# Kernel optimization log

Measured on AMD Instinct MI355X. Metric: run time of the kernel, lower is better.

The kernel has to match this reference:

```python
import jax, jax.numpy as jnp
import numpy as np

B, S, H = 8, 8192, 1024
CAPACITY_FACTOR = 0.5


def setup_inputs() -> dict:
    key = jax.random.key(0)
    ks = jax.random.split(key, 5)
    sc = lambda fan: np.float32(1.0 / np.sqrt(fan))
    return {
        "x": jax.random.normal(ks[0], (B, S, H), dtype=jnp.float32),
        # router: Linear(H, H//4) -> ReLU -> Linear(H//4, 1)
        "W1": jax.random.normal(ks[1], (H, H // 4), dtype=jnp.float32) * sc(H),
        "b1": jnp.zeros((H // 4,), dtype=jnp.float32),
        "W2": jax.random.normal(ks[2], (H // 4, 1), dtype=jnp.float32) * sc(H // 4),
        "b2": jnp.zeros((1,), dtype=jnp.float32),
        # external layer_fn realized as a dense layer: gelu(x @ Wl)
        "Wl": jax.random.normal(ks[3], (H, H), dtype=jnp.float32) * sc(H),
    }


def reference(x, W1, b1, W2, b2, Wl):
    # router scores [B, S, 1]
    scores = jax.nn.relu(jnp.einsum("bsh,hd->bsd", x, W1) + b1)
    scores = jnp.einsum("bsd,do->bso", scores, W2) + b2
    routing_weights = jax.nn.sigmoid(scores)  # [B, S, 1]

    # eval path: process only top-capacity tokens per batch row
    capacity = int(S * CAPACITY_FACTOR)
    _, top_idx = jax.lax.top_k(scores[..., 0], capacity)  # [B, C]

    selected = jnp.take_along_axis(x, top_idx[..., None], axis=1)  # [B, C, H]
    processed = jax.nn.gelu(jnp.einsum("bch,hd->bcd", selected, Wl))  # layer_fn

    batch_idx = jnp.arange(x.shape[0])[:, None]  # [B, 1]
    output = x.at[batch_idx, top_idx].set(processed)  # scatter back into clone of x
    return output, routing_weights
```

## Files before the change

kernel.cpp:

```cpp
#include <hip/hip_runtime.h>
#include <stdint.h>

#define B_   8
#define S_   8192
#define H_   1024
#define HQ_  256
#define CAP_ 4096
#define UCAP_ (S_-CAP_)
#define M_   (B_*CAP_)
#define EPSB 0.012f
#define LCAP 8192

using f32x4 = __attribute__((ext_vector_type(4))) float;
using s16x8 = __attribute__((ext_vector_type(8))) short;

__device__ __forceinline__ unsigned short f2bf(float f) {
  unsigned u = __float_as_uint(f);
  u += 0x7FFF + ((u >> 16) & 1);
  return (unsigned short)(u >> 16);
}
__device__ __forceinline__ float bf2f(unsigned short h) {
  return __uint_as_float(((unsigned)h) << 16);
}

__device__ __forceinline__ float gelu_f(float v) {
  float s = v + 0.044715f * v * v * v;
  float e = __expf(-1.5957691216057308f * s);
  return v * __builtin_amdgcn_rcpf(1.0f + e);
}

__device__ __forceinline__ unsigned mono(float f) {
  unsigned u = __float_as_uint(f);
  return (u & 0x80000000u) ? ~u : (u | 0x80000000u);
}
__device__ __forceinline__ float unmono(unsigned k) {
  unsigned u = (k & 0x80000000u) ? (k & 0x7fffffffu) : ~k;
  return __uint_as_float(u);
}

__device__ __forceinline__ void gload_lds16(const void* g, void* l) {
  __builtin_amdgcn_global_load_lds(
      (const __attribute__((address_space(1))) void*)(uintptr_t)g,
      (__attribute__((address_space(3))) void*)(uintptr_t)l,
      16, 0, 0);
}

__global__ __launch_bounds__(256) void prep_w1_kernel(
    const float* __restrict__ W1, unsigned short* __restrict__ w1t_hi) {
  __shared__ float tile[32][33];
  const int n0 = blockIdx.x * 32, k0 = blockIdx.y * 32;
  const int tx = threadIdx.x, ty = threadIdx.y;
  for (int i = ty; i < 32; i += 8) tile[i][tx] = W1[(size_t)(k0 + i) * HQ_ + n0 + tx];
  __syncthreads();
  for (int i = ty; i < 32; i += 8)
    w1t_hi[(size_t)(n0 + i) * H_ + k0 + tx] = f2bf(tile[tx][i]);
}

__global__ __launch_bounds__(512) void router_mfma_kernel(
    const float* __restrict__ x, const unsigned short* __restrict__ w1t_hi,
    const float* __restrict__ b1, const float* __restrict__ W2,
    const float* __restrict__ b2, float* __restrict__ scores) {
  __shared__ __align__(16) unsigned short AsH[128 * 32];
  __shared__ __align__(16) unsigned short BsH[256 * 32];
  __shared__ float part[128][4];
  const int t = threadIdx.x;
  const int lane = t & 63, w = t >> 6;
  const int m0 = blockIdx.x * 128;
  const int wr = w >> 2, wc = w & 3;
  const int r16 = lane & 15, ks = lane >> 4;

  f32x4 acc[4][4];
  #pragma unroll
  for (int i = 0; i < 4; ++i)
    #pragma unroll
    for (int j = 0; j < 4; ++j) acc[i][j] = (f32x4){0.f, 0.f, 0.f, 0.f};

  for (int k0 = 0; k0 < H_; k0 += 32) {
    #pragma unroll
    for (int u = 0; u < 2; ++u) {
      int idx = t + u * 512;
      int row = idx >> 3, q = idx & 7;
      float4 v = *(const float4*)&x[(size_t)(m0 + row) * H_ + k0 + q * 4];
      ushort4 hh;
      hh.x = f2bf(v.x); hh.y = f2bf(v.y); hh.z = f2bf(v.z); hh.w = f2bf(v.w);
      int so = row * 32 + (((q >> 1) ^ (row & 3)) << 3) + (q & 1) * 4;
      *(ushort4*)&AsH[so] = hh;
    }
    {
      int c0 = w * 64;
      #pragma unroll
      for (int q = 0; q < 2; ++q) {
        int cc0 = (q * 8 + w) * 64;
        int g = cc0 + lane;
        int row = g >> 2, sl = g & 3;
        int slz = sl ^ (row & 3);
        gload_lds16(&w1t_hi[(size_t)row * H_ + k0 + slz * 8], &BsH[cc0 * 8]);
      }
      (void)c0;
    }
    __syncthreads();
    s16x8 ah[4], bh[4];
    #pragma unroll
    for (int i = 0; i < 4; ++i) {
      int r = wr * 64 + i * 16 + r16;
      int co = (ks ^ (r & 3)) * 8;
      ah[i] = *(const s16x8*)&AsH[r * 32 + co];
    }
    #pragma unroll
    for (int j = 0; j < 4; ++j) {
      int r = wc * 64 + j * 16 + r16;
      int co = (ks ^ (r & 3)) * 8;
      bh[j] = *(const s16x8*)&BsH[r * 32 + co];
    }
    #pragma unroll
    for (int i = 0; i < 4; ++i)
      #pragma unroll
      for (int j = 0; j < 4; ++j)
        acc[i][j] = __builtin_amdgcn_mfma_f32_16x16x32_bf16(ah[i], bh[j], acc[i][j], 0, 0, 0);
    __syncthreads();
  }

  float b1v[4], w2v[4];
  #pragma unroll
  for (int j = 0; j < 4; ++j) {
    int n = wc * 64 + j * 16 + r16;
    b1v[j] = b1[n]; w2v[j] = W2[n];
  }
  const int g4 = lane >> 4;
  #pragma unroll
  for (int i = 0; i < 4; ++i) {
    #pragma unroll
    for (int r = 0; r < 4; ++r) {
      float p = 0.f;
      #pragma unroll
      for (int j = 0; j < 4; ++j) {
        float h = acc[i][j][r] + b1v[j];
        h = fmaxf(h, 0.f);
        p = fmaf(h, w2v[j], p);
      }
      p += __shfl_xor(p, 1);
      p += __shfl_xor(p, 2);
      p += __shfl_xor(p, 4);
      p += __shfl_xor(p, 8);
      if (r16 == 0) part[wr * 64 + i * 16 + g4 * 4 + r][wc] = p;
    }
  }
  __syncthreads();
  if (t < 128)
    scores[m0 + t] = part[t][0] + part[t][1] + part[t][2] + part[t][3] + b2[0];
}

__global__ __launch_bounds__(1024) void select_kernel(
    const float* __restrict__ scores, float* __restrict__ thr) {
  __shared__ unsigned hist[2048];
  __shared__ unsigned sh_b, sh_gt;
  const int b = blockIdx.x;
  const int tid = threadIdx.x;
  const float* srow = scores + (size_t)b * S_;
  unsigned prefix = 0; int plen = 0; unsigned rank = CAP_;
  #pragma unroll
  for (int round = 0; round < 3; ++round) {
    const int nb = (round < 2) ? 11 : 10;
    hist[tid] = 0; hist[tid + 1024] = 0;
    __syncthreads();
    for (int i = tid; i < S_; i += 1024) {
      unsigned k = mono(srow[i]);
      if (plen == 0 || (k >> (32 - plen)) == prefix) {
        unsigned bucket = (k << plen) >> (32 - nb);
        atomicAdd(&hist[bucket], 1u);
      }
    }
    __syncthreads();
    for (int s = 1; s < 2048; s <<= 1) {
      unsigned t0 = (tid + s < 2048) ? hist[tid + s] : 0;
      unsigned t1 = (tid + 1024 + s < 2048) ? hist[tid + 1024 + s] : 0;
      __syncthreads();
      hist[tid] += t0; hist[tid + 1024] += t1;
      __syncthreads();
    }
    #pragma unroll
    for (int h = 0; h < 2; ++h) {
      int i = tid + h * 1024;
      unsigned ge = hist[i];
      unsigned gt = (i < 2047) ? hist[i + 1] : 0;
      if (gt < rank && rank <= ge) { sh_b = (unsigned)i; sh_gt = gt; }
    }
    __syncthreads();
    prefix = (prefix << nb) | sh_b;
    plen += nb;
    rank -= sh_gt;
    __syncthreads();
  }
  if (tid == 0) thr[b] = unmono(prefix);
}

__global__ __launch_bounds__(256) void band_kernel(
    const float* __restrict__ scores, const float* __restrict__ thr,
    int* __restrict__ list, int* __restrict__ count) {
  int i = blockIdx.x * 256 + threadIdx.x;
  float s = scores[i];
  int b = i >> 13;
  if (fabsf(s - thr[b]) <= EPSB) {
    int p = atomicAdd(count, 1);
    if (p < LCAP) list[p] = i;
  }
}

__global__ __launch_bounds__(256) void recompute_kernel(
    const float* __restrict__ x, const float* __restrict__ W1,
    const float* __restrict__ b1, const float* __restrict__ W2,
    const float* __restrict__ b2, const int* __restrict__ list,
    const int* __restrict__ count, float* __restrict__ scores) {
  __shared__ float xr[4][H_];
  __shared__ float red[4][4];
  int n = *count; if (n > LCAP) n = LCAP;
  const int j = threadIdx.x;
  for (int base = blockIdx.x * 4; base < n; base += gridDim.x * 4) {
    int nt = n - base; if (nt > 4) nt = 4;
    for (int tt = 0; tt < 4; ++tt) {
      int tok = list[base + ((tt < nt) ? tt : 0)];
      const float* xrow = x + (size_t)tok * H_;
      for (int k = j; k < H_; k += 256) xr[tt][k] = xrow[k];
    }
    __syncthreads();
    float a0 = 0.f, a1 = 0.f, a2 = 0.f, a3 = 0.f;
    for (int k = 0; k < H_; ++k) {
      float wv = W1[(size_t)k * HQ_ + j];
      a0 = fmaf(xr[0][k], wv, a0);
      a1 = fmaf(xr[1][k], wv, a1);
      a2 = fmaf(xr[2][k], wv, a2);
      a3 = fmaf(xr[3][k], wv, a3);
    }
    float aa[4] = {a0, a1, a2, a3};
    #pragma unroll
    for (int tt = 0; tt < 4; ++tt) {
      float h = fmaxf(aa[tt] + b1[j], 0.f);
      float v = h * W2[j];
      v += __shfl_xor(v, 1);  v += __shfl_xor(v, 2);  v += __shfl_xor(v, 4);
      v += __shfl_xor(v, 8);  v += __shfl_xor(v, 16); v += __shfl_xor(v, 32);
      if ((j & 63) == 0) red[tt][j >> 6] = v;
    }
    __syncthreads();
    if (j < nt)
      scores[list[base + j]] = red[j][0] + red[j][1] + red[j][2] + red[j][3] + b2[0];
    __syncthreads();
  }
}

__global__ __launch_bounds__(1024) void compact_kernel(
    const float* __restrict__ scores, const float* __restrict__ thr,
    int* __restrict__ comp, int* __restrict__ ucomp) {
  __shared__ int wc_eq[16], wc_sel[16], red[16];
  const int b = blockIdx.x;
  const float T = thr[b];
  const float* srow = scores + (size_t)b * S_;
  const int tid = threadIdx.x, lane = tid & 63, wid = tid >> 6;

  int cgt = 0;
  #pragma unroll
  for (int c = 0; c < 8; ++c) cgt += (srow[c * 1024 + tid] > T) ? 1 : 0;
  cgt += __shfl_xor(cgt, 1);  cgt += __shfl_xor(cgt, 2);  cgt += __shfl_xor(cgt, 4);
  cgt += __shfl_xor(cgt, 8);  cgt += __shfl_xor(cgt, 16); cgt += __shfl_xor(cgt, 32);
  if (lane == 0) red[wid] = cgt;
  __syncthreads();
  int cnt_gt = 0;
  #pragma unroll
  for (int i = 0; i < 16; ++i) cnt_gt += red[i];
  const int need = CAP_ - cnt_gt;

  int* crow = comp + b * CAP_;
  int* urow = ucomp + b * UCAP_;
  int sel_base = 0, unsel_base = 0, eq_base = 0;
  __syncthreads();
  for (int c = 0; c < 8; ++c) {
    int idx = c * 1024 + tid;
    float s = srow[idx];
    bool gt = s > T, eq = (s == T);
    unsigned long long meq = __ballot(eq);
    if (lane == 0) wc_eq[wid] = __popcll(meq);
    __syncthreads();
    int eq_off = eq_base, eq_tot = 0;
    #pragma unroll
    for (int w2 = 0; w2 < 16; ++w2) { if (w2 < wid) eq_off += wc_eq[w2]; eq_tot += wc_eq[w2]; }
    int eqpos = eq_off + __popcll(meq & ((1ull << lane) - 1));
    bool take = gt || (eq && eqpos < need);
    unsigned long long mt = __ballot(take);
    if (lane == 0) wc_sel[wid] = __popcll(mt);
    __syncthreads();
    int sel_off = sel_base, sel_tot = 0;
    #pragma unroll
    for (int w2 = 0; w2 < 16; ++w2) { if (w2 < wid) sel_off += wc_sel[w2]; sel_tot += wc_sel[w2]; }
    if (take) {
      crow[sel_off + __popcll(mt & ((1ull << lane) - 1))] = idx;
    } else {
      int un_off = unsel_base + wid * 64 - (sel_off - sel_base);
      urow[un_off + __popcll(~mt & ((1ull << lane) - 1))] = idx;
    }
    sel_base += sel_tot; unsel_base += 1024 - sel_tot; eq_base += eq_tot;
    __syncthreads();
  }
}

__global__ __launch_bounds__(256) void rw_kernel(
    const float* __restrict__ scores, float* __restrict__ rw) {
  int i = blockIdx.x * 256 + threadIdx.x;
  rw[i] = 1.f / (1.f + expf(-scores[i]));
}

__global__ __launch_bounds__(256) void copy_unsel_kernel(
    const float* __restrict__ x, const int* __restrict__ ucomp,
    float* __restrict__ out) {
  int i = blockIdx.x;
  int b = i >> 12, r = i & (UCAP_ - 1);
  int token = ucomp[b * UCAP_ + r];
  size_t row = (size_t)b * S_ + token;
  const float4* src = (const float4*)(x + row * H_);
  float4* dst = (float4*)(out + row * H_);
  dst[threadIdx.x] = src[threadIdx.x];
}

__global__ __launch_bounds__(256) void wlt_kernel(
    const float* __restrict__ wl, unsigned short* __restrict__ wlt) {
  __shared__ float tile[32][33];
  const int x0 = blockIdx.x * 32, y0 = blockIdx.y * 32;
  const int tx = threadIdx.x, ty = threadIdx.y;
  for (int i = ty; i < 32; i += 8) tile[i][tx] = wl[(size_t)(y0 + i) * H_ + x0 + tx];
  __syncthreads();
  for (int i = ty; i < 32; i += 8)
    wlt[(size_t)(x0 + i) * H_ + y0 + tx] = f2bf(tile[tx][i]);
}

__global__ __launch_bounds__(256) void gather_cast_kernel(
    const float* __restrict__ x, const int* __restrict__ comp,
    unsigned short* __restrict__ xg) {
  int tid = blockIdx.x * 256 + threadIdx.x;
  int rowc = tid >> 8;
  int c4 = tid & 255;
  int b = rowc >> 12, cc = rowc & (CAP_ - 1);
  int token = comp[b * CAP_ + cc];
  float4 v = *(const float4*)&x[((size_t)(b * S_ + token)) * H_ + c4 * 4];
  ushort4 o;
  o.x = f2bf(v.x); o.y = f2bf(v.y); o.z = f2bf(v.z); o.w = f2bf(v.w);
  *(ushort4*)&xg[(size_t)rowc * H_ + c4 * 4] = o;
}

__global__ __launch_bounds__(256) void moe_gemm_kernel(
    const unsigned short* __restrict__ xg, const unsigned short* __restrict__ wlt,
    const int* __restrict__ comp, float* __restrict__ out) {
  __shared__ __align__(16) unsigned short As[128 * 64];
  __shared__ __align__(16) unsigned short Bs[128 * 64];
  __shared__ int toks[128];
  const int t = threadIdx.x;
  const int lane = t & 63, w = t >> 6;
  const int bid = blockIdx.x;
  const int xcd = bid & 7, wl_ = bid >> 3;
  const int m0 = (xcd * 32 + (wl_ >> 3)) * 128;
  const int n0 = (wl_ & 7) * 128;
  const int bb = m0 >> 12;
  if (t < 128) toks[t] = comp[bb * CAP_ + (m0 & (CAP_ - 1)) + t];
  const int wr = w >> 1, wc = w & 1;
  const int r16 = lane & 15, ks = lane >> 4;

  const unsigned short* aS[4];
  const unsigned short* bS[4];
  #pragma unroll
  for (int u = 0; u < 4; ++u) {
    int c = u * 256 + t;
    int row = c >> 3, sl = c & 7;
    int slz = sl ^ (row & 7);
    aS[u] = xg + (size_t)(m0 + row) * H_ + slz * 8;
    bS[u] = wlt + (size_t)(n0 + row) * H_ + slz * 8;
  }

  f32x4 acc[4][4];
  #pragma unroll
  for (int i = 0; i < 4; ++i)
    #pragma unroll
    for (int j = 0; j < 4; ++j) acc[i][j] = (f32x4){0.f, 0.f, 0.f, 0.f};

  for (int k0 = 0; k0 < H_; k0 += 64) {
    #pragma unroll
    for (int u = 0; u < 4; ++u) {
      gload_lds16(aS[u] + k0, &As[(u * 256 + w * 64) * 8]);
      gload_lds16(bS[u] + k0, &Bs[(u * 256 + w * 64) * 8]);
    }
    __syncthreads();
    #pragma unroll
    for (int kk = 0; kk < 2; ++kk) {
      s16x8 af[4], bfr[4];
      const int g = kk * 4 + ks;
      #pragma unroll
      for (int i = 0; i < 4; ++i) {
        int r = wr * 64 + i * 16 + r16;
        af[i] = *(const s16x8*)&As[r * 64 + (g ^ (r & 7)) * 8];
      }
      #pragma unroll
      for (int j = 0; j < 4; ++j) {
        int r = wc * 64 + j * 16 + r16;
        bfr[j] = *(const s16x8*)&Bs[r * 64 + (g ^ (r & 7)) * 8];
      }
      #pragma unroll
      for (int i = 0; i < 4; ++i)
        #pragma unroll
        for (int j = 0; j < 4; ++j)
          acc[i][j] = __builtin_amdgcn_mfma_f32_16x16x32_bf16(af[i], bfr[j], acc[i][j], 0, 0, 0);
    }
    __syncthreads();
  }

  #pragma unroll
  for (int i = 0; i < 4; ++i) {
    #pragma unroll
    for (int r = 0; r < 4; ++r) {
      int rl = wr * 64 + i * 16 + (lane >> 4) * 4 + r;
      int token = toks[rl];
      float* orow = out + ((size_t)(bb * S_ + token)) * H_ + n0 + wc * 64;
      #pragma unroll
      for (int j = 0; j < 4; ++j)
        orow[j * 16 + r16] = gelu_f(acc[i][j][r]);
    }
  }
}

extern "C" void kernel_launch(void* const* d_in, const int* in_sizes, int n_in,
                              void* d_out, int out_size, void* d_ws, size_t ws_size,
                              hipStream_t stream) {
  const float* x  = (const float*)d_in[0];
  const float* W1 = (const float*)d_in[1];
  const float* b1 = (const float*)d_in[2];
  const float* W2 = (const float*)d_in[3];
  const float* b2 = (const float*)d_in[4];
  const float* Wl = (const float*)d_in[5];
  float* out = (float*)d_out;
  float* rw  = out + (size_t)B_ * S_ * H_;

  char* ws = (char*)d_ws;
  float* scores        = (float*)ws;
  int*   comp          = (int*)(ws + (256 << 10));
  float* thr           = (float*)(ws + (384 << 10));
  int*   count         = (int*)(ws + (384 << 10) + 256);
  int*   list          = (int*)(ws + (384 << 10) + 512);
  int*   ucomp         = (int*)(ws + (448 << 10));
  unsigned short* wlt  = (unsigned short*)(ws + (1 << 20));
  unsigned short* xg   = (unsigned short*)(ws + (3 << 20));
  unsigned short* w1t_hi = xg;

  hipMemsetAsync(count, 0, sizeof(int), stream);
  hipLaunchKernelGGL(prep_w1_kernel, dim3(HQ_/32, H_/32), dim3(32, 8), 0, stream,
                     W1, w1t_hi);
  hipLaunchKernelGGL(router_mfma_kernel, dim3((B_*S_)/128), dim3(512), 0, stream,
                     x, w1t_hi, b1, W2, b2, scores);
  hipLaunchKernelGGL(select_kernel, dim3(B_), dim3(1024), 0, stream, scores, thr);
  hipLaunchKernelGGL(band_kernel, dim3((B_*S_)/256), dim3(256), 0, stream,
                     scores, thr, list, count);
  hipLaunchKernelGGL(recompute_kernel, dim3(128), dim3(256), 0, stream,
                     x, W1, b1, W2, b2, list, count, scores);
  hipLaunchKernelGGL(select_kernel, dim3(B_), dim3(1024), 0, stream, scores, thr);
  hipLaunchKernelGGL(compact_kernel, dim3(B_), dim3(1024), 0, stream,
                     scores, thr, comp, ucomp);
  hipLaunchKernelGGL(rw_kernel, dim3((B_*S_)/256), dim3(256), 0, stream,
                     scores, rw);
  hipLaunchKernelGGL(copy_unsel_kernel, dim3(B_*UCAP_), dim3(256), 0, stream,
                     x, ucomp, out);
  hipLaunchKernelGGL(wlt_kernel, dim3(H_/32, H_/32), dim3(32, 8), 0, stream, Wl, wlt);
  hipLaunchKernelGGL(gather_cast_kernel, dim3(M_*H_/4/256), dim3(256), 0, stream,
                     x, comp, xg);
  hipLaunchKernelGGL(moe_gemm_kernel, dim3((M_/128)*(H_/128)), dim3(256), 0, stream,
                     xg, wlt, comp, out);
}
```

Baseline: 441.4 us.

## Double-buffer router and MoE GEMM LDS tiles and fuse sigmoid into router

Both the router GEMM and the MoE GEMM now use two LDS buffers, so the next K-tile's global loads are issued before the MFMAs on the current tile and one barrier per iteration is removed. The MoE GEMM K-tile shrinks from 64 to 32 so the doubled buffers fit in the same LDS footprint. The sigmoid routing-weight computation moves into the router and recompute kernels, which removes a separate launch and one pass over the scores. The shorter K-step means twice as many loop iterations and barriers in the MoE GEMM, and double buffering raises LDS and register pressure, which may lower occupancy.

```diff
diff --git a/kernel.cpp b/kernel.cpp
--- a/kernel.cpp
+++ b/kernel.cpp
@@ -59,9 +59,10 @@
 __global__ __launch_bounds__(512) void router_mfma_kernel(
     const float* __restrict__ x, const unsigned short* __restrict__ w1t_hi,
     const float* __restrict__ b1, const float* __restrict__ W2,
-    const float* __restrict__ b2, float* __restrict__ scores) {
-  __shared__ __align__(16) unsigned short AsH[128 * 32];
-  __shared__ __align__(16) unsigned short BsH[256 * 32];
+    const float* __restrict__ b2, float* __restrict__ scores,
+    float* __restrict__ rw) {
+  __shared__ __align__(16) unsigned short AsH[2][128 * 32];
+  __shared__ __align__(16) unsigned short BsH[2][256 * 32];
   __shared__ float part[128][4];
   const int t = threadIdx.x;
   const int lane = t & 63, w = t >> 6;
@@ -69,54 +70,85 @@
   const int wr = w >> 2, wc = w & 3;
   const int r16 = lane & 15, ks = lane >> 4;
 
+  const float* aptr[2];
+  int aso[2];
+  #pragma unroll
+  for (int u = 0; u < 2; ++u) {
+    int idx = t + u * 512;
+    int row = idx >> 3, q = idx & 7;
+    aptr[u] = x + (size_t)(m0 + row) * H_ + q * 4;
+    aso[u] = row * 32 + (((q >> 1) ^ (row & 3)) << 3) + (q & 1) * 4;
+  }
+  const unsigned short* bptr[2];
+  int bdst[2];
+  #pragma unroll
+  for (int q = 0; q < 2; ++q) {
+    int cc0 = (q * 8 + w) * 64;
+    int g = cc0 + lane;
+    int row = g >> 2, sl = g & 3;
+    int slz = sl ^ (row & 3);
+    bptr[q] = w1t_hi + (size_t)row * H_ + slz * 8;
+    bdst[q] = cc0 * 8;
+  }
+
   f32x4 acc[4][4];
   #pragma unroll
   for (int i = 0; i < 4; ++i)
     #pragma unroll
     for (int j = 0; j < 4; ++j) acc[i][j] = (f32x4){0.f, 0.f, 0.f, 0.f};
 
-  for (int k0 = 0; k0 < H_; k0 += 32) {
+  {
+    float4 av[2];
+    #pragma unroll
+    for (int u = 0; u < 2; ++u) av[u] = *(const float4*)(aptr[u]);
+    #pragma unroll
+    for (int q = 0; q < 2; ++q) gload_lds16(bptr[q], &BsH[0][bdst[q]]);
     #pragma unroll
     for (int u = 0; u < 2; ++u) {
-      int idx = t + u * 512;
-      int row = idx >> 3, q = idx & 7;
-      float4 v = *(const float4*)&x[(size_t)(m0 + row) * H_ + k0 + q * 4];
       ushort4 hh;
-      hh.x = f2bf(v.x); hh.y = f2bf(v.y); hh.z = f2bf(v.z); hh.w = f2bf(v.w);
-      int so = row * 32 + (((q >> 1) ^ (row & 3)) << 3) + (q & 1) * 4;
-      *(ushort4*)&AsH[so] = hh;
-    }
-    {
-      int c0 = w * 64;
-      #pragma unroll
-      for (int q = 0; q < 2; ++q) {
-        int cc0 = (q * 8 + w) * 64;
-        int g = cc0 + lane;
-        int row = g >> 2, sl = g & 3;
-        int slz = sl ^ (row & 3);
-        gload_lds16(&w1t_hi[(size_t)row * H_ + k0 + slz * 8], &BsH[cc0 * 8]);
-      }
-      (void)c0;
-    }
-    __syncthreads();
+      hh.x = f2bf(av[u].x); hh.y = f2bf(av[u].y);
+      hh.z = f2bf(av[u].z); hh.w = f2bf(av[u].w);
+      *(ushort4*)&AsH[0][aso[u]] = hh;
+    }
+    __syncthreads();
+  }
+
+  for (int kt = 0; kt < 32; ++kt) {
+    const int cur = kt & 1;
+    const int k1 = (kt + 1) * 32;
+    const bool pf = (kt < 31);
+    float4 av[2];
+    if (pf) {
+      #pragma unroll
+      for (int u = 0; u < 2; ++u) av[u] = *(const float4*)(aptr[u] + k1);
+      #pragma unroll
+      for (int q = 0; q < 2; ++q) gload_lds16(bptr[q] + k1, &BsH[cur ^ 1][bdst[q]]);
+    }
     s16x8 ah[4], bh[4];
     #pragma unroll
     for (int i = 0; i < 4; ++i) {
       int r = wr * 64 + i * 16 + r16;
-      int co = (ks ^ (r & 3)) * 8;
-      ah[i] = *(const s16x8*)&AsH[r * 32 + co];
+      ah[i] = *(const s16x8*)&AsH[cur][r * 32 + (ks ^ (r & 3)) * 8];
     }
     #pragma unroll
     for (int j = 0; j < 4; ++j) {
       int r = wc * 64 + j * 16 + r16;
-      int co = (ks ^ (r & 3)) * 8;
-      bh[j] = *(const s16x8*)&BsH[r * 32 + co];
+      bh[j] = *(const s16x8*)&BsH[cur][r * 32 + (ks ^ (r & 3)) * 8];
     }
     #pragma unroll
     for (int i = 0; i < 4; ++i)
       #pragma unroll
       for (int j = 0; j < 4; ++j)
         acc[i][j] = __builtin_amdgcn_mfma_f32_16x16x32_bf16(ah[i], bh[j], acc[i][j], 0, 0, 0);
+    if (pf) {
+      #pragma unroll
+      for (int u = 0; u < 2; ++u) {
+        ushort4 hh;
+        hh.x = f2bf(av[u].x); hh.y = f2bf(av[u].y);
+        hh.z = f2bf(av[u].z); hh.w = f2bf(av[u].w);
+        *(ushort4*)&AsH[cur ^ 1][aso[u]] = hh;
+      }
+    }
     __syncthreads();
   }
 
@@ -146,8 +178,11 @@
     }
   }
   __syncthreads();
-  if (t < 128)
-    scores[m0 + t] = part[t][0] + part[t][1] + part[t][2] + part[t][3] + b2[0];
+  if (t < 128) {
+    float sc = part[t][0] + part[t][1] + part[t][2] + part[t][3] + b2[0];
+    scores[m0 + t] = sc;
+    rw[m0 + t] = 1.f / (1.f + expf(-sc));
+  }
 }
 
 __global__ __launch_bounds__(1024) void select_kernel(
@@ -210,7 +245,8 @@
     const float* __restrict__ x, const float* __restrict__ W1,
     const float* __restrict__ b1, const float* __restrict__ W2,
     const float* __restrict__ b2, const int* __restrict__ list,
-    const int* __restrict__ count, float* __restrict__ scores) {
+    const int* __restrict__ count, float* __restrict__ scores,
+    float* __restrict__ rw) {
   __shared__ float xr[4][H_];
   __shared__ float red[4][4];
   int n = *count; if (n > LCAP) n = LCAP;
@@ -241,8 +277,12 @@
       if ((j & 63) == 0) red[tt][j >> 6] = v;
     }
     __syncthreads();
-    if (j < nt)
-      scores[list[base + j]] = red[j][0] + red[j][1] + red[j][2] + red[j][3] + b2[0];
+    if (j < nt) {
+      int tok = list[base + j];
+      float sc = red[j][0] + red[j][1] + red[j][2] + red[j][3] + b2[0];
+      scores[tok] = sc;
+      rw[tok] = 1.f / (1.f + expf(-sc));
+    }
     __syncthreads();
   }
 }
@@ -299,12 +339,6 @@
     sel_base += sel_tot; unsel_base += 1024 - sel_tot; eq_base += eq_tot;
     __syncthreads();
   }
-}
-
-__global__ __launch_bounds__(256) void rw_kernel(
-    const float* __restrict__ scores, float* __restrict__ rw) {
-  int i = blockIdx.x * 256 + threadIdx.x;
-  rw[i] = 1.f / (1.f + expf(-scores[i]));
 }
 
 __global__ __launch_bounds__(256) void copy_unsel_kernel(
@@ -347,8 +381,8 @@
 __global__ __launch_bounds__(256) void moe_gemm_kernel(
     const unsigned short* __restrict__ xg, const unsigned short* __restrict__ wlt,
     const int* __restrict__ comp, float* __restrict__ out) {
-  __shared__ __align__(16) unsigned short As[128 * 64];
-  __shared__ __align__(16) unsigned short Bs[128 * 64];
+  __shared__ __align__(16) unsigned short As[2][128 * 32];
+  __shared__ __align__(16) unsigned short Bs[2][128 * 32];
   __shared__ int toks[128];
   const int t = threadIdx.x;
   const int lane = t & 63, w = t >> 6;
@@ -361,15 +395,16 @@
   const int wr = w >> 1, wc = w & 1;
   const int r16 = lane & 15, ks = lane >> 4;
 
-  const unsigned short* aS[4];
-  const unsigned short* bS[4];
-  #pragma unroll
-  for (int u = 0; u < 4; ++u) {
+  const unsigned short *aP[2], *bP[2];
+  int dst[2];
+  #pragma unroll
+  for (int u = 0; u < 2; ++u) {
     int c = u * 256 + t;
-    int row = c >> 3, sl = c & 7;
-    int slz = sl ^ (row & 7);
-    aS[u] = xg + (size_t)(m0 + row) * H_ + slz * 8;
-    bS[u] = wlt + (size_t)(n0 + row) * H_ + slz * 8;
+    int row = c >> 2, sl = c & 3;
+    int slz = sl ^ (row & 3);
+    aP[u] = xg + (size_t)(m0 + row) * H_ + slz * 8;
+    bP[u] = wlt + (size_t)(n0 + row) * H_ + slz * 8;
+    dst[u] = (u * 256 + w * 64) * 8;
   }
 
   f32x4 acc[4][4];
@@ -378,33 +413,39 @@
     #pragma unroll
     for (int j = 0; j < 4; ++j) acc[i][j] = (f32x4){0.f, 0.f, 0.f, 0.f};
 
-  for (int k0 = 0; k0 < H_; k0 += 64) {
-    #pragma unroll
-    for (int u = 0; u < 4; ++u) {
-      gload_lds16(aS[u] + k0, &As[(u * 256 + w * 64) * 8]);
-      gload_lds16(bS[u] + k0, &Bs[(u * 256 + w * 64) * 8]);
-    }
-    __syncthreads();
-    #pragma unroll
-    for (int kk = 0; kk < 2; ++kk) {
-      s16x8 af[4], bfr[4];
-      const int g = kk * 4 + ks;
-      #pragma unroll
-      for (int i = 0; i < 4; ++i) {
-        int r = wr * 64 + i * 16 + r16;
-        af[i] = *(const s16x8*)&As[r * 64 + (g ^ (r & 7)) * 8];
+  #pragma unroll
+  for (int u = 0; u < 2; ++u) {
+    gload_lds16(aP[u], &As[0][dst[u]]);
+    gload_lds16(bP[u], &Bs[0][dst[u]]);
+  }
+  __syncthreads();
+
+  for (int kt = 0; kt < 32; ++kt) {
+    const int cur = kt & 1;
+    const int k1 = (kt + 1) * 32;
+    if (kt < 31) {
+      #pragma unroll
+      for (int u = 0; u < 2; ++u) {
+        gload_lds16(aP[u] + k1, &As[cur ^ 1][dst[u]]);
+        gload_lds16(bP[u] + k1, &Bs[cur ^ 1][dst[u]]);
       }
-      #pragma unroll
-      for (int j = 0; j < 4; ++j) {
-        int r = wc * 64 + j * 16 + r16;
-        bfr[j] = *(const s16x8*)&Bs[r * 64 + (g ^ (r & 7)) * 8];
-      }
-      #pragma unroll
-      for (int i = 0; i < 4; ++i)
-        #pragma unroll
-        for (int j = 0; j < 4; ++j)
-          acc[i][j] = __builtin_amdgcn_mfma_f32_16x16x32_bf16(af[i], bfr[j], acc[i][j], 0, 0, 0);
-    }
+    }
+    s16x8 af[4], bfr[4];
+    #pragma unroll
+    for (int i = 0; i < 4; ++i) {
+      int r = wr * 64 + i * 16 + r16;
+      af[i] = *(const s16x8*)&As[cur][r * 32 + (ks ^ (r & 3)) * 8];
+    }
+    #pragma unroll
+    for (int j = 0; j < 4; ++j) {
+      int r = wc * 64 + j * 16 + r16;
+      bfr[j] = *(const s16x8*)&Bs[cur][r * 32 + (ks ^ (r & 3)) * 8];
+    }
+    #pragma unroll
+    for (int i = 0; i < 4; ++i)
+      #pragma unroll
+      for (int j = 0; j < 4; ++j)
+        acc[i][j] = __builtin_amdgcn_mfma_f32_16x16x32_bf16(af[i], bfr[j], acc[i][j], 0, 0, 0);
     __syncthreads();
   }
 
@@ -449,17 +490,15 @@
   hipLaunchKernelGGL(prep_w1_kernel, dim3(HQ_/32, H_/32), dim3(32, 8), 0, stream,
                      W1, w1t_hi);
   hipLaunchKernelGGL(router_mfma_kernel, dim3((B_*S_)/128), dim3(512), 0, stream,
-                     x, w1t_hi, b1, W2, b2, scores);
+                     x, w1t_hi, b1, W2, b2, scores, rw);
   hipLaunchKernelGGL(select_kernel, dim3(B_), dim3(1024), 0, stream, scores, thr);
   hipLaunchKernelGGL(band_kernel, dim3((B_*S_)/256), dim3(256), 0, stream,
                      scores, thr, list, count);
   hipLaunchKernelGGL(recompute_kernel, dim3(128), dim3(256), 0, stream,
-                     x, W1, b1, W2, b2, list, count, scores);
+                     x, W1, b1, W2, b2, list, count, scores, rw);
   hipLaunchKernelGGL(select_kernel, dim3(B_), dim3(1024), 0, stream, scores, thr);
   hipLaunchKernelGGL(compact_kernel, dim3(B_), dim3(1024), 0, stream,
                      scores, thr, comp, ucomp);
-  hipLaunchKernelGGL(rw_kernel, dim3((B_*S_)/256), dim3(256), 0, stream,
-                     scores, rw);
   hipLaunchKernelGGL(copy_unsel_kernel, dim3(B_*UCAP_), dim3(256), 0, stream,
                      x, ucomp, out);
   hipLaunchKernelGGL(wlt_kernel, dim3(H_/32, H_/32), dim3(32, 8), 0, stream, Wl, wlt);
```

Measured after the change: 427.7 us. 1.03x faster.

## Double router GEMM K-tile to 64, precompute load addresses, fuse sigmoid into router

Applied to the files above, without the earlier changes.

The router GEMM now stages a 64-wide K slice per iteration instead of 32, with an 8-way XOR swizzle and two MFMA sub-steps per tile. This halves the number of barrier pairs and loop iterations over K, and all global loads are issued before the bf16 conversion. Per-thread global and LDS addresses are computed once, outside the loop. The sigmoid routing weight is written directly by the router and recompute kernels, which removes the separate rw_kernel launch and its extra pass over scores. In exchange, LDS use doubles and register pressure rises.

```diff
diff --git a/kernel.cpp b/kernel.cpp
--- a/kernel.cpp
+++ b/kernel.cpp
@@ -59,9 +59,10 @@
 __global__ __launch_bounds__(512) void router_mfma_kernel(
     const float* __restrict__ x, const unsigned short* __restrict__ w1t_hi,
     const float* __restrict__ b1, const float* __restrict__ W2,
-    const float* __restrict__ b2, float* __restrict__ scores) {
-  __shared__ __align__(16) unsigned short AsH[128 * 32];
-  __shared__ __align__(16) unsigned short BsH[256 * 32];
+    const float* __restrict__ b2, float* __restrict__ scores,
+    float* __restrict__ rw) {
+  __shared__ __align__(16) unsigned short AsH[128 * 64];
+  __shared__ __align__(16) unsigned short BsH[256 * 64];
   __shared__ float part[128][4];
   const int t = threadIdx.x;
   const int lane = t & 63, w = t >> 6;
@@ -69,54 +70,67 @@
   const int wr = w >> 2, wc = w & 3;
   const int r16 = lane & 15, ks = lane >> 4;
 
+  const float* aptr[4];
+  int aso[4];
+  #pragma unroll
+  for (int u = 0; u < 4; ++u) {
+    int idx = t + u * 512;
+    int row = idx >> 4, q = idx & 15;
+    aptr[u] = x + (size_t)(m0 + row) * H_ + q * 4;
+    aso[u] = row * 64 + (((q >> 1) ^ (row & 7)) << 3) + (q & 1) * 4;
+  }
+  const unsigned short* bptr[4];
+  int bdst[4];
+  #pragma unroll
+  for (int u = 0; u < 4; ++u) {
+    int c0 = u * 512 + w * 64;
+    int c = c0 + lane;
+    int row = c >> 3, sl = c & 7;
+    int slz = sl ^ (row & 7);
+    bptr[u] = w1t_hi + (size_t)row * H_ + slz * 8;
+    bdst[u] = c0 * 8;
+  }
+
   f32x4 acc[4][4];
   #pragma unroll
   for (int i = 0; i < 4; ++i)
     #pragma unroll
     for (int j = 0; j < 4; ++j) acc[i][j] = (f32x4){0.f, 0.f, 0.f, 0.f};
 
-  for (int k0 = 0; k0 < H_; k0 += 32) {
-    #pragma unroll
-    for (int u = 0; u < 2; ++u) {
-      int idx = t + u * 512;
-      int row = idx >> 3, q = idx & 7;
-      float4 v = *(const float4*)&x[(size_t)(m0 + row) * H_ + k0 + q * 4];
+  for (int k0 = 0; k0 < H_; k0 += 64) {
+    float4 av[4];
+    #pragma unroll
+    for (int u = 0; u < 4; ++u) av[u] = *(const float4*)(aptr[u] + k0);
+    #pragma unroll
+    for (int u = 0; u < 4; ++u) gload_lds16(bptr[u] + k0, &BsH[bdst[u]]);
+    #pragma unroll
+    for (int u = 0; u < 4; ++u) {
       ushort4 hh;
-      hh.x = f2bf(v.x); hh.y = f2bf(v.y); hh.z = f2bf(v.z); hh.w = f2bf(v.w);
-      int so = row * 32 + (((q >> 1) ^ (row & 3)) << 3) + (q & 1) * 4;
-      *(ushort4*)&AsH[so] = hh;
-    }
-    {
-      int c0 = w * 64;
-      #pragma unroll
-      for (int q = 0; q < 2; ++q) {
-        int cc0 = (q * 8 + w) * 64;
-        int g = cc0 + lane;
-        int row = g >> 2, sl = g & 3;
-        int slz = sl ^ (row & 3);
-        gload_lds16(&w1t_hi[(size_t)row * H_ + k0 + slz * 8], &BsH[cc0 * 8]);
-      }
-      (void)c0;
-    }
-    __syncthreads();
-    s16x8 ah[4], bh[4];
-    #pragma unroll
-    for (int i = 0; i < 4; ++i) {
-      int r = wr * 64 + i * 16 + r16;
-      int co = (ks ^ (r & 3)) * 8;
-      ah[i] = *(const s16x8*)&AsH[r * 32 + co];
-    }
-    #pragma unroll
-    for (int j = 0; j < 4; ++j) {
-      int r = wc * 64 + j * 16 + r16;
-      int co = (ks ^ (r & 3)) * 8;
-      bh[j] = *(const s16x8*)&BsH[r * 32 + co];
-    }
-    #pragma unroll
-    for (int i = 0; i < 4; ++i)
-      #pragma unroll
-      for (int j = 0; j < 4; ++j)
-        acc[i][j] = __builtin_amdgcn_mfma_f32_16x16x32_bf16(ah[i], bh[j], acc[i][j], 0, 0, 0);
+      hh.x = f2bf(av[u].x); hh.y = f2bf(av[u].y);
+      hh.z = f2bf(av[u].z); hh.w = f2bf(av[u].w);
+      *(ushort4*)&AsH[aso[u]] = hh;
+    }
+    __syncthreads();
+    #pragma unroll
+    for (int kk = 0; kk < 2; ++kk) {
+      const int g = kk * 4 + ks;
+      s16x8 ah[4], bh[4];
+      #pragma unroll
+      for (int i = 0; i < 4; ++i) {
+        int r = wr * 64 + i * 16 + r16;
+        ah[i] = *(const s16x8*)&AsH[r * 64 + (g ^ (r & 7)) * 8];
+      }
+      #pragma unroll
+      for (int j = 0; j < 4; ++j) {
+        int r = wc * 64 + j * 16 + r16;
+        bh[j] = *(const s16x8*)&BsH[r * 64 + (g ^ (r & 7)) * 8];
+      }
+      #pragma unroll
+      for (int i = 0; i < 4; ++i)
+        #pragma unroll
+        for (int j = 0; j < 4; ++j)
+          acc[i][j] = __builtin_amdgcn_mfma_f32_16x16x32_bf16(ah[i], bh[j], acc[i][j], 0, 0, 0);
+    }
     __syncthreads();
   }
 
@@ -146,8 +160,11 @@
     }
   }
   __syncthreads();
-  if (t < 128)
-    scores[m0 + t] = part[t][0] + part[t][1] + part[t][2] + part[t][3] + b2[0];
+  if (t < 128) {
+    float sc = part[t][0] + part[t][1] + part[t][2] + part[t][3] + b2[0];
+    scores[m0 + t] = sc;
+    rw[m0 + t] = 1.f / (1.f + expf(-sc));
+  }
 }
 
 __global__ __launch_bounds__(1024) void select_kernel(
@@ -210,7 +227,8 @@
     const float* __restrict__ x, const float* __restrict__ W1,
     const float* __restrict__ b1, const float* __restrict__ W2,
     const float* __restrict__ b2, const int* __restrict__ list,
-    const int* __restrict__ count, float* __restrict__ scores) {
+    const int* __restrict__ count, float* __restrict__ scores,
+    float* __restrict__ rw) {
   __shared__ float xr[4][H_];
   __shared__ float red[4][4];
   int n = *count; if (n > LCAP) n = LCAP;
@@ -241,8 +259,12 @@
       if ((j & 63) == 0) red[tt][j >> 6] = v;
     }
     __syncthreads();
-    if (j < nt)
-      scores[list[base + j]] = red[j][0] + red[j][1] + red[j][2] + red[j][3] + b2[0];
+    if (j < nt) {
+      int tok = list[base + j];
+      float sc = red[j][0] + red[j][1] + red[j][2] + red[j][3] + b2[0];
+      scores[tok] = sc;
+      rw[tok] = 1.f / (1.f + expf(-sc));
+    }
     __syncthreads();
   }
 }
@@ -299,12 +321,6 @@
     sel_base += sel_tot; unsel_base += 1024 - sel_tot; eq_base += eq_tot;
     __syncthreads();
   }
-}
-
-__global__ __launch_bounds__(256) void rw_kernel(
-    const float* __restrict__ scores, float* __restrict__ rw) {
-  int i = blockIdx.x * 256 + threadIdx.x;
-  rw[i] = 1.f / (1.f + expf(-scores[i]));
 }
 
 __global__ __launch_bounds__(256) void copy_unsel_kernel(
@@ -449,17 +465,15 @@
   hipLaunchKernelGGL(prep_w1_kernel, dim3(HQ_/32, H_/32), dim3(32, 8), 0, stream,
                      W1, w1t_hi);
   hipLaunchKernelGGL(router_mfma_kernel, dim3((B_*S_)/128), dim3(512), 0, stream,
-                     x, w1t_hi, b1, W2, b2, scores);
+                     x, w1t_hi, b1, W2, b2, scores, rw);
   hipLaunchKernelGGL(select_kernel, dim3(B_), dim3(1024), 0, stream, scores, thr);
   hipLaunchKernelGGL(band_kernel, dim3((B_*S_)/256), dim3(256), 0, stream,
                      scores, thr, list, count);
   hipLaunchKernelGGL(recompute_kernel, dim3(128), dim3(256), 0, stream,
-                     x, W1, b1, W2, b2, list, count, scores);
+                     x, W1, b1, W2, b2, list, count, scores, rw);
   hipLaunchKernelGGL(select_kernel, dim3(B_), dim3(1024), 0, stream, scores, thr);
   hipLaunchKernelGGL(compact_kernel, dim3(B_), dim3(1024), 0, stream,
                      scores, thr, comp, ucomp);
-  hipLaunchKernelGGL(rw_kernel, dim3((B_*S_)/256), dim3(256), 0, stream,
-                     scores, rw);
   hipLaunchKernelGGL(copy_unsel_kernel, dim3(B_*UCAP_), dim3(256), 0, stream,
                      x, ucomp, out);
   hipLaunchKernelGGL(wlt_kernel, dim3(H_/32, H_/32), dim3(32, 8), 0, stream, Wl, wlt);
```

Result: no change. 434.1 us (-1.7%).
